# Kernel optimization log

Hardware: AMD Instinct MI355X
Metric: run time of the kernel (lower is better)

## Reference

```python
import jax, jax.numpy as jnp
import numpy as np

NUM_ITERS = 2      # num_iters default
NEG_SLOPE = 0.2    # LeakyReLU slope in GAT attention
NEG_INF = -1e9

N, E, B, H, K, L = 204800, 6144000, 4096, 8, 30, 50


def setup_inputs() -> dict:
    key = jax.random.key(0)
    ks = jax.random.split(key, 14)
    return {
        "target_features": jax.random.normal(ks[0], (N, 8), jnp.float32),
        "feature_dist_graph": jax.random.normal(ks[1], (E, 8), jnp.float32),
        "rij_dist_pairs": jax.random.uniform(ks[2], (E,), jnp.float32),
        "b_scope": jax.random.randint(ks[3], (N, K), 0, E + 1, jnp.int32),
        "start_end_env": jax.random.randint(ks[4], (N, K), 0, N + 1, jnp.int32),
        "l_scope": jax.random.randint(ks[5], (B, L), 0, N + 1, jnp.int32),
        "edge_src": jax.random.randint(ks[6], (E,), 0, N + 1, jnp.int32),
        "W_emb": jax.random.normal(ks[7], (8, H), jnp.float32),
        "b_emb": jax.random.normal(ks[8], (H,), jnp.float32),
        "W_dist": jax.random.normal(ks[9], (9, H), jnp.float32),
        "b_dist": jax.random.normal(ks[10], (H,), jnp.float32),
        "W_gat": jax.random.normal(ks[11], (H, H), jnp.float32),
        "a_src": jax.random.normal(ks[12], (H,), jnp.float32),
        "a_dst": jax.random.normal(ks[13], (H,), jnp.float32),
    }


def reference(target_features, feature_dist_graph, rij_dist_pairs,
              b_scope, start_end_env, l_scope, edge_src,
              W_emb, b_emb, W_dist, b_dist, W_gat, a_src, a_dst):
    # node embedding: [N, 8] -> [N, H]
    h = target_features @ W_emb + b_emb
    # edge (feature+distance) embedding: [E, 9] -> [E, H]
    msg = jnp.concatenate([feature_dist_graph, rij_dist_pairs[:, None]], axis=1) @ W_dist + b_dist
    zero = jnp.zeros((1, h.shape[1]), h.dtype)
    h = jnp.concatenate([zero, h], axis=0)          # zero row for 1-based / padded indices
    pad_mask = b_scope > 0                           # padded neighbor slots point at row 0
    for _ in range(NUM_ITERS):
        nbr_self = h[start_end_env]                  # getConnectedFeatures: [N, K, H] (target repeated)
        msg0 = jnp.concatenate([zero, msg], axis=0)  # zero row for padded edge indices
        nbr_msg = msg0[b_scope]                      # gathered neighbor messages [N, K, H]
        # GAT attention over the K neighbor slots
        z_s = nbr_self @ W_gat                       # [N, K, H]
        z_m = nbr_msg @ W_gat                        # [N, K, H]
        e = jax.nn.leaky_relu(z_s @ a_src + z_m @ a_dst, NEG_SLOPE)  # [N, K]
        e = jnp.where(pad_mask, e, NEG_INF)
        alpha = jax.nn.softmax(e, axis=1)            # [N, K]
        out = jnp.einsum('nk,nkh->nh', alpha, z_m)   # attention-weighted aggregate [N, H]
        h = jnp.concatenate([zero, jax.nn.elu(out)], axis=0)  # [N+1, H]
        # updateConnectedDict: scatter node states back to per-edge messages
        msg = h[edge_src]                            # [E, H]
    # readout: gather per-graph feature rows and sum -> mol_vecs [B, H]
    return h[l_scope].sum(axis=1)
```

## Files before the change

### kernel.cpp

```cpp
#include <hip/hip_runtime.h>

typedef float f32x4 __attribute__((ext_vector_type(4)));

#define NEG_SLOPE 0.2f
#define NEG_INF   -1e9f

__global__ void prep_embed(const float* __restrict__ fdg,
                           const float* __restrict__ rij,
                           const int* __restrict__ b_scope,
                           const int* __restrict__ edge_src,
                           const float* __restrict__ W_dist,
                           const float* __restrict__ b_dist,
                           const float* __restrict__ W_gat,
                           const float* __restrict__ a_src,
                           const float* __restrict__ tf,
                           const float* __restrict__ W_emb,
                           const float* __restrict__ b_emb,
                           float* __restrict__ rec,
                           int* __restrict__ src_idx,
                           float* __restrict__ h_a,
                           float* __restrict__ h_b,
                           float* __restrict__ t0,
                           float* __restrict__ t1,
                           int E, int NK, int N,
                           int nb_pair, int nb_edge, int nb_slot) {
    __shared__ float sW[72];
    __shared__ float sb[8];
    __shared__ float sWg[64];
    __shared__ float s_vec[8];
    int tid = threadIdx.x;
    int bid = blockIdx.x;

    int type, widx;
    if (bid < 2 * nb_pair) {
        type = bid & 1;
        widx = bid >> 1;
    } else {
        int r = bid - 2 * nb_pair;
        if (r < nb_edge - nb_pair)      { type = 0; widx = nb_pair + r; }
        else {
            r -= (nb_edge - nb_pair);
            if (r < nb_slot - nb_pair)  { type = 1; widx = nb_pair + r; }
            else                        { type = 2; widx = r - (nb_slot - nb_pair); }
        }
    }

    if (type == 0) {
        if (tid < 72) sW[tid] = W_dist[tid];
        else if (tid < 80) sb[tid - 72] = b_dist[tid - 72];
    } else if (type == 2) {
        if (tid < 64) sW[tid] = W_emb[tid];
        else if (tid < 72) sb[tid - 64] = b_emb[tid - 64];
        if (tid >= 128 && tid < 192) sWg[tid - 128] = W_gat[tid - 128];
    }
    __syncthreads();
    if (type == 2 && tid < 8) {
        float s = 0.f;
        #pragma unroll
        for (int j = 0; j < 8; ++j) s += sWg[tid * 8 + j] * a_src[j];
        s_vec[tid] = s;
    }
    __syncthreads();

    if (type == 0) {
        int e = widx * 256 + tid;
        if (e >= E) return;
        const f32x4* fr = reinterpret_cast<const f32x4*>(fdg + (size_t)e * 8);
        f32x4 g0 = fr[0], g1 = fr[1];
        float rv = rij[e];
        float msg[8];
        #pragma unroll
        for (int j = 0; j < 8; ++j) {
            float s = sb[j];
            #pragma unroll
            for (int i = 0; i < 4; ++i) s += g0[i] * sW[i * 8 + j];
            #pragma unroll
            for (int i = 0; i < 4; ++i) s += g1[i] * sW[(4 + i) * 8 + j];
            s += rv * sW[64 + j];
            msg[j] = s;
        }
        f32x4* op = reinterpret_cast<f32x4*>(rec + (size_t)e * 8);
        f32x4 m0 = {msg[0], msg[1], msg[2], msg[3]};
        f32x4 m1 = {msg[4], msg[5], msg[6], msg[7]};
        op[0] = m0; op[1] = m1;
    } else if (type == 1) {
        int s = widx * 256 + tid;
        if (s >= NK) return;
        int bs = b_scope[s];
        src_idx[s] = (bs > 0) ? edge_src[bs - 1] : -1;
    } else {
        int n = widx * 256 + tid;
        if (n >= N) return;
        if (n == 0) {
            #pragma unroll
            for (int j = 0; j < 8; ++j) { h_a[j] = 0.f; h_b[j] = 0.f; }
            t0[0] = 0.f;
            t1[0] = 0.f;
        }
        const f32x4* tfr = reinterpret_cast<const f32x4*>(tf + (size_t)n * 8);
        f32x4 a = tfr[0], b = tfr[1];
        float x[8] = {a[0], a[1], a[2], a[3], b[0], b[1], b[2], b[3]};
        float out[8];
        #pragma unroll
        for (int j = 0; j < 8; ++j) out[j] = sb[j];
        #pragma unroll
        for (int i = 0; i < 8; ++i)
            #pragma unroll
            for (int j = 0; j < 8; ++j)
                out[j] += x[i] * sW[i * 8 + j];
        float t = 0.f;
        #pragma unroll
        for (int p = 0; p < 8; ++p) t += out[p] * s_vec[p];
        t0[n + 1] = t;
        f32x4* hr = reinterpret_cast<f32x4*>(h_a + (size_t)(n + 1) * 8);
        f32x4 o0 = {out[0], out[1], out[2], out[3]};
        f32x4 o1 = {out[4], out[5], out[6], out[7]};
        hr[0] = o0;
        hr[1] = o1;
    }
}

__device__ __forceinline__ void finish_node(const float msg[8], float t_se, float em,
                                            bool has, bool vk, int lane, int node,
                                            const float* __restrict__ sWg,
                                            const float* __restrict__ s_as,
                                            float* __restrict__ h_next,
                                            float* __restrict__ t_next) {
    float ee = t_se + em;
    ee = (ee >= 0.f) ? ee : NEG_SLOPE * ee;
    float e = has ? ee : (vk ? NEG_INF : -3e38f);

    float m = e;
    #pragma unroll
    for (int off = 16; off; off >>= 1) m = fmaxf(m, __shfl_xor(m, off, 32));
    float p = vk ? expf(e - m) : 0.f;
    float denom = p;
    #pragma unroll
    for (int off = 16; off; off >>= 1) denom += __shfl_xor(denom, off, 32);
    float alpha = p / denom;

    float agg[8];
    #pragma unroll
    for (int j = 0; j < 8; ++j) agg[j] = alpha * msg[j];
    #pragma unroll
    for (int off = 16; off; off >>= 1)
        #pragma unroll
        for (int j = 0; j < 8; ++j) agg[j] += __shfl_xor(agg[j], off, 32);

    if (lane < 8) {
        float o = 0.f;
        #pragma unroll
        for (int i = 0; i < 8; ++i) o += agg[i] * sWg[i * 8 + lane];
        o = (o > 0.f) ? o : (expf(o) - 1.f);
        h_next[(size_t)(node + 1) * 8 + lane] = o;
        if (t_next) {
            float tv = o * s_as[lane];
            tv += __shfl_xor(tv, 1, 32);
            tv += __shfl_xor(tv, 2, 32);
            tv += __shfl_xor(tv, 4, 32);
            if (lane == 0) t_next[node + 1] = tv;
        }
    }
}

__global__ void gat_iter1_rec(const float* __restrict__ t0,
                              float* __restrict__ h1,
                              float* __restrict__ t1,
                              const int* __restrict__ b_scope,
                              const int* __restrict__ se_env,
                              const float* __restrict__ rec,
                              const float* __restrict__ W_gat,
                              const float* __restrict__ a_src,
                              const float* __restrict__ a_dst,
                              int N, int K) {
    __shared__ float sWg[64];
    __shared__ float s_as[8];
    __shared__ float s_ad[8];
    int tid = threadIdx.x;
    if (tid < 64) sWg[tid] = W_gat[tid];
    __syncthreads();
    if (tid < 8) {
        float s = 0.f;
        #pragma unroll
        for (int j = 0; j < 8; ++j) s += sWg[tid * 8 + j] * a_src[j];
        s_as[tid] = s;
    } else if (tid < 16) {
        int i = tid - 8;
        float s = 0.f;
        #pragma unroll
        for (int j = 0; j < 8; ++j) s += sWg[i * 8 + j] * a_dst[j];
        s_ad[i] = s;
    }
    __syncthreads();

    int node = blockIdx.x * 8 + (tid >> 5);
    int lane = tid & 31;
    if (node >= N) return;
    bool vk = (lane < K);

    int bs = 0, se = 0;
    if (vk) {
        bs = b_scope[(size_t)node * K + lane];
        se = se_env[(size_t)node * K + lane];
    }
    bool has = vk && (bs > 0);
    float t_se = vk ? t0[se] : 0.f;

    f32x4 m0 = {0,0,0,0}, m1 = {0,0,0,0};
    if (has) {
        const f32x4* rp = reinterpret_cast<const f32x4*>(rec + (size_t)(bs - 1) * 8);
        m0 = rp[0]; m1 = rp[1];
    }
    float msg[8] = {m0[0], m0[1], m0[2], m0[3], m1[0], m1[1], m1[2], m1[3]};
    float em = 0.f;
    #pragma unroll
    for (int j = 0; j < 8; ++j) em += msg[j] * s_ad[j];

    finish_node(msg, t_se, em, has, vk, lane, node, sWg, s_as, h1, t1);
}

__global__ void gat_iter1_fb(const float* __restrict__ t0,
                             float* __restrict__ h1,
                             float* __restrict__ t1,
                             const int* __restrict__ b_scope,
                             const int* __restrict__ se_env,
                             const float* __restrict__ fdg,
                             const float* __restrict__ rij,
                             const float* __restrict__ W_dist,
                             const float* __restrict__ b_dist,
                             const float* __restrict__ W_gat,
                             const float* __restrict__ a_src,
                             const float* __restrict__ a_dst,
                             int N, int K) {
    __shared__ float sWg[64];
    __shared__ float s_as[8];
    __shared__ float s_ad[8];
    __shared__ float sWd[72];
    __shared__ float sbd[8];
    int tid = threadIdx.x;
    if (tid < 64) sWg[tid] = W_gat[tid];
    if (tid >= 64 && tid < 136) sWd[tid - 64] = W_dist[tid - 64];
    if (tid >= 136 && tid < 144) sbd[tid - 136] = b_dist[tid - 136];
    __syncthreads();
    if (tid < 8) {
        float s = 0.f;
        #pragma unroll
        for (int j = 0; j < 8; ++j) s += sWg[tid * 8 + j] * a_src[j];
        s_as[tid] = s;
    } else if (tid < 16) {
        int i = tid - 8;
        float s = 0.f;
        #pragma unroll
        for (int j = 0; j < 8; ++j) s += sWg[i * 8 + j] * a_dst[j];
        s_ad[i] = s;
    }
    __syncthreads();

    int node = blockIdx.x * 8 + (tid >> 5);
    int lane = tid & 31;
    if (node >= N) return;
    bool vk = (lane < K);

    int bs = 0, se = 0;
    if (vk) {
        bs = b_scope[(size_t)node * K + lane];
        se = se_env[(size_t)node * K + lane];
    }
    bool has = vk && (bs > 0);
    float t_se = vk ? t0[se] : 0.f;

    float msg[8];
    #pragma unroll
    for (int j = 0; j < 8; ++j) msg[j] = 0.f;
    float em = 0.f;
    if (has) {
        const f32x4* fr = reinterpret_cast<const f32x4*>(fdg + (size_t)(bs - 1) * 8);
        f32x4 g0 = fr[0], g1 = fr[1];
        float rv = rij[bs - 1];
        #pragma unroll
        for (int j = 0; j < 8; ++j) {
            float s = sbd[j];
            #pragma unroll
            for (int i = 0; i < 4; ++i) s += g0[i] * sWd[i * 8 + j];
            #pragma unroll
            for (int i = 0; i < 4; ++i) s += g1[i] * sWd[(4 + i) * 8 + j];
            s += rv * sWd[64 + j];
            msg[j] = s;
        }
        #pragma unroll
        for (int j = 0; j < 8; ++j) em += msg[j] * s_ad[j];
    }
    finish_node(msg, t_se, em, has, vk, lane, node, sWg, s_as, h1, t1);
}

template <bool SRCIDX>
__global__ void gat_iter2(const float* __restrict__ h1,
                          const float* __restrict__ t1,
                          float* __restrict__ h2,
                          const int* __restrict__ src_idx,
                          const int* __restrict__ b_scope,
                          const int* __restrict__ se_env,
                          const int* __restrict__ edge_src,
                          const float* __restrict__ W_gat,
                          const float* __restrict__ a_dst,
                          int N, int K) {
    __shared__ float sWg[64];
    __shared__ float s_ad[8];
    int tid = threadIdx.x;
    if (tid < 64) sWg[tid] = W_gat[tid];
    __syncthreads();
    if (tid < 8) {
        float s = 0.f;
        #pragma unroll
        for (int j = 0; j < 8; ++j) s += sWg[tid * 8 + j] * a_dst[j];
        s_ad[tid] = s;
    }
    __syncthreads();

    int lane = tid & 31;
    int g = blockIdx.x * 8 + (tid >> 5);
    int nA = g * 2, nB = g * 2 + 1;
    if (nA >= N) return;
    bool hasBn = (nB < N);
    bool vk = (lane < K);

    int srcA = -1, srcB = -1, seA = 0, seB = 0;
    if (SRCIDX) {
        if (vk) {
            srcA = src_idx[(size_t)nA * K + lane];
            seA  = se_env[(size_t)nA * K + lane];
            if (hasBn) {
                srcB = src_idx[(size_t)nB * K + lane];
                seB  = se_env[(size_t)nB * K + lane];
            }
        }
    } else {
        int bsA = 0, bsB = 0;
        if (vk) {
            bsA = b_scope[(size_t)nA * K + lane];
            seA = se_env[(size_t)nA * K + lane];
            if (hasBn) {
                bsB = b_scope[(size_t)nB * K + lane];
                seB = se_env[(size_t)nB * K + lane];
            }
        }
        if (vk && bsA > 0) srcA = edge_src[bsA - 1];
        if (vk && hasBn && bsB > 0) srcB = edge_src[bsB - 1];
    }
    bool hasA = vk && (srcA >= 0);
    bool hasB = vk && hasBn && (srcB >= 0);

    float tA = vk ? t1[seA] : 0.f;
    float tB = (vk && hasBn) ? t1[seB] : 0.f;

    f32x4 a0 = {0,0,0,0}, a1 = {0,0,0,0}, b0 = {0,0,0,0}, b1 = {0,0,0,0};
    if (hasA) {
        const f32x4* mr = reinterpret_cast<const f32x4*>(h1 + (size_t)srcA * 8);
        a0 = mr[0]; a1 = mr[1];
    }
    if (hasB) {
        const f32x4* mr = reinterpret_cast<const f32x4*>(h1 + (size_t)srcB * 8);
        b0 = mr[0]; b1 = mr[1];
    }

    float msgA[8] = {a0[0], a0[1], a0[2], a0[3], a1[0], a1[1], a1[2], a1[3]};
    float emA = 0.f;
    #pragma unroll
    for (int j = 0; j < 8; ++j) emA += msgA[j] * s_ad[j];
    finish_node(msgA, tA, emA, hasA, vk, lane, nA, sWg, nullptr, h2, nullptr);
    if (hasBn) {
        float msgB[8] = {b0[0], b0[1], b0[2], b0[3], b1[0], b1[1], b1[2], b1[3]};
        float emB = 0.f;
        #pragma unroll
        for (int j = 0; j < 8; ++j) emB += msgB[j] * s_ad[j];
        finish_node(msgB, tB, emB, hasB, vk, lane, nB, sWg, nullptr, h2, nullptr);
    }
}

__global__ void readout_kernel(const float* __restrict__ h,
                               const int* __restrict__ l_scope,
                               float* __restrict__ out, int B, int L) {
    int gid = blockIdx.x * blockDim.x + threadIdx.x;
    int b = gid >> 3;
    int j = gid & 7;
    if (b >= B) return;
    float s = 0.f;
    for (int l = 0; l < L; ++l) {
        int idx = l_scope[(size_t)b * L + l];
        s += h[(size_t)idx * 8 + j];
    }
    out[(size_t)b * 8 + j] = s;
}

extern "C" void kernel_launch(void* const* d_in, const int* in_sizes, int n_in,
                              void* d_out, int out_size, void* d_ws, size_t ws_size,
                              hipStream_t stream) {
    const float* tf      = (const float*)d_in[0];
    const float* fdg     = (const float*)d_in[1];
    const float* rij     = (const float*)d_in[2];
    const int* b_scope   = (const int*)d_in[3];
    const int* start_env = (const int*)d_in[4];
    const int* l_scope   = (const int*)d_in[5];
    const int* edge_src  = (const int*)d_in[6];
    const float* W_emb   = (const float*)d_in[7];
    const float* b_emb   = (const float*)d_in[8];
    const float* W_dist  = (const float*)d_in[9];
    const float* b_dist  = (const float*)d_in[10];
    const float* W_gat   = (const float*)d_in[11];
    const float* a_src   = (const float*)d_in[12];
    const float* a_dst   = (const float*)d_in[13];
    float* out = (float*)d_out;

    const int N = in_sizes[0] / 8;
    const int E = in_sizes[1] / 8;
    const int K = in_sizes[3] / N;
    const int L = 50;
    const int B = in_sizes[5] / L;
    const int NK = N * K;

    size_t rec_f = (size_t)E * 8;
    size_t need  = (rec_f + (size_t)NK
                    + 2 * (size_t)(N + 1) * 8 + 2 * (size_t)(N + 1)) * 4;
    bool use_rec = (ws_size >= need);

    float* base = (float*)d_ws;
    float* rec  = base;
    size_t off  = use_rec ? rec_f : 0;
    float* h_a  = base + off;  off += (size_t)(N + 1) * 8;
    float* h_b  = base + off;  off += (size_t)(N + 1) * 8;
    float* t0v  = base + off;  off += (size_t)(N + 1);
    float* t1v  = base + off;  off += (size_t)(N + 1);
    int* src_idx = (int*)(base + off);

    const int nb_edge = (E + 255) / 256;
    const int nb_slot = (NK + 255) / 256;
    const int nb_node = (N + 255) / 256;
    const int nb_pair = (nb_edge < nb_slot) ? nb_edge : nb_slot;

    if (use_rec) {
        const int grid = nb_edge + nb_slot + nb_node;
        prep_embed<<<grid, 256, 0, stream>>>(
            fdg, rij, b_scope, edge_src, W_dist, b_dist, W_gat, a_src,
            tf, W_emb, b_emb, rec, src_idx, h_a, h_b, t0v, t1v,
            E, NK, N, nb_pair, nb_edge, nb_slot);
        gat_iter1_rec<<<(N + 7) / 8, 256, 0, stream>>>(t0v, h_b, t1v,
                                                       b_scope, start_env, rec,
                                                       W_gat, a_src, a_dst, N, K);
        const int g2_blocks = ((N + 1) / 2 + 7) / 8;
        gat_iter2<true><<<g2_blocks, 256, 0, stream>>>(h_b, t1v, h_a,
                                                       src_idx, b_scope, start_env,
                                                       edge_src, W_gat, a_dst, N, K);
    } else {
        prep_embed<<<nb_node, 256, 0, stream>>>(
            fdg, rij, b_scope, edge_src, W_dist, b_dist, W_gat, a_src,
            tf, W_emb, b_emb, rec, (int*)rec, h_a, h_b, t0v, t1v,
            0, 0, N, 0, 0, 0);
        gat_iter1_fb<<<(N + 7) / 8, 256, 0, stream>>>(t0v, h_b, t1v,
                                                      b_scope, start_env,
                                                      fdg, rij,
                                                      W_dist, b_dist, W_gat,
                                                      a_src, a_dst, N, K);
        const int g2_blocks = ((N + 1) / 2 + 7) / 8;
        gat_iter2<false><<<g2_blocks, 256, 0, stream>>>(h_b, t1v, h_a,
                                                        (const int*)rec, b_scope, start_env,
                                                        edge_src, W_gat, a_dst, N, K);
    }

    readout_kernel<<<(B * 8 + 255) / 256, 256, 0, stream>>>(h_a, l_scope, out, B, L);
}
```

Measured before the change: 406.8 us.

## Split each neighbor slot across two lanes in a 64-wide wavefront per node

The GAT iteration kernels now use a full 64-lane wavefront per node, with two lanes per neighbor slot. Each lane loads one 16-byte half of the gathered 8-float message row, and the halves are exchanged with a shuffle. The aim is to spread the random gather loads across more lanes and to use wave64 natively instead of 32-lane sub-groups. In exchange, the reductions gain an extra shuffle step, half the lanes do duplicate softmax work, and the two-nodes-per-warp batching in iteration 2 is dropped.

```diff
diff --git a/kernel.cpp b/kernel.cpp
--- a/kernel.cpp
+++ b/kernel.cpp
@@ -120,45 +120,45 @@
     }
 }
 
-__device__ __forceinline__ void finish_node(const float msg[8], float t_se, float em,
-                                            bool has, bool vk, int lane, int node,
+__device__ __forceinline__ void finish_pair(const float msg[8], float t_se, float em,
+                                            bool own, bool has, int k, int h, int node,
                                             const float* __restrict__ sWg,
                                             const float* __restrict__ s_as,
                                             float* __restrict__ h_next,
                                             float* __restrict__ t_next) {
     float ee = t_se + em;
     ee = (ee >= 0.f) ? ee : NEG_SLOPE * ee;
-    float e = has ? ee : (vk ? NEG_INF : -3e38f);
+    float e = own ? (has ? ee : NEG_INF) : -3e38f;
 
     float m = e;
     #pragma unroll
-    for (int off = 16; off; off >>= 1) m = fmaxf(m, __shfl_xor(m, off, 32));
-    float p = vk ? expf(e - m) : 0.f;
+    for (int off = 32; off >= 2; off >>= 1) m = fmaxf(m, __shfl_xor(m, off, 64));
+    float p = own ? expf(e - m) : 0.f;
     float denom = p;
     #pragma unroll
-    for (int off = 16; off; off >>= 1) denom += __shfl_xor(denom, off, 32);
+    for (int off = 32; off >= 2; off >>= 1) denom += __shfl_xor(denom, off, 64);
     float alpha = p / denom;
 
     float agg[8];
     #pragma unroll
     for (int j = 0; j < 8; ++j) agg[j] = alpha * msg[j];
     #pragma unroll
-    for (int off = 16; off; off >>= 1)
-        #pragma unroll
-        for (int j = 0; j < 8; ++j) agg[j] += __shfl_xor(agg[j], off, 32);
-
-    if (lane < 8) {
+    for (int off = 32; off >= 2; off >>= 1)
+        #pragma unroll
+        for (int j = 0; j < 8; ++j) agg[j] += __shfl_xor(agg[j], off, 64);
+
+    if (h == 0 && k < 8) {
         float o = 0.f;
         #pragma unroll
-        for (int i = 0; i < 8; ++i) o += agg[i] * sWg[i * 8 + lane];
+        for (int i = 0; i < 8; ++i) o += agg[i] * sWg[i * 8 + k];
         o = (o > 0.f) ? o : (expf(o) - 1.f);
-        h_next[(size_t)(node + 1) * 8 + lane] = o;
+        h_next[(size_t)(node + 1) * 8 + k] = o;
         if (t_next) {
-            float tv = o * s_as[lane];
-            tv += __shfl_xor(tv, 1, 32);
-            tv += __shfl_xor(tv, 2, 32);
-            tv += __shfl_xor(tv, 4, 32);
-            if (lane == 0) t_next[node + 1] = tv;
+            float tv = o * s_as[k];
+            tv += __shfl_xor(tv, 2, 64);
+            tv += __shfl_xor(tv, 4, 64);
+            tv += __shfl_xor(tv, 8, 64);
+            if (k == 0) t_next[node + 1] = tv;
         }
     }
 }
@@ -193,30 +193,132 @@
     }
     __syncthreads();
 
-    int node = blockIdx.x * 8 + (tid >> 5);
-    int lane = tid & 31;
+    int node = blockIdx.x * 4 + (tid >> 6);
+    int lane = tid & 63;
+    int k = lane >> 1;
+    int h = lane & 1;
     if (node >= N) return;
-    bool vk = (lane < K);
+    bool vk  = (k < K);
+    bool own = vk && (h == 0);
 
     int bs = 0, se = 0;
     if (vk) {
-        bs = b_scope[(size_t)node * K + lane];
-        se = se_env[(size_t)node * K + lane];
+        bs = b_scope[(size_t)node * K + k];
+        se = se_env[(size_t)node * K + k];
     }
     bool has = vk && (bs > 0);
-    float t_se = vk ? t0[se] : 0.f;
-
-    f32x4 m0 = {0,0,0,0}, m1 = {0,0,0,0};
-    if (has) {
-        const f32x4* rp = reinterpret_cast<const f32x4*>(rec + (size_t)(bs - 1) * 8);
-        m0 = rp[0]; m1 = rp[1];
-    }
-    float msg[8] = {m0[0], m0[1], m0[2], m0[3], m1[0], m1[1], m1[2], m1[3]};
+
+    f32x4 mh = {0, 0, 0, 0};
+    if (has)
+        mh = *reinterpret_cast<const f32x4*>(rec + (size_t)(bs - 1) * 8 + h * 4);
+    float t_se = own ? t0[se] : 0.f;
+
+    f32x4 m1;
+    #pragma unroll
+    for (int c = 0; c < 4; ++c) m1[c] = __shfl(mh[c], lane | 1, 64);
+    float msg[8] = {mh[0], mh[1], mh[2], mh[3], m1[0], m1[1], m1[2], m1[3]};
+
     float em = 0.f;
     #pragma unroll
     for (int j = 0; j < 8; ++j) em += msg[j] * s_ad[j];
 
-    finish_node(msg, t_se, em, has, vk, lane, node, sWg, s_as, h1, t1);
+    finish_pair(msg, t_se, em, own, has, k, h, node, sWg, s_as, h1, t1);
+}
+
+__global__ void gat_iter2_pair(const float* __restrict__ h1,
+                               const float* __restrict__ t1,
+                               float* __restrict__ h2,
+                               const int* __restrict__ src_idx,
+                               const int* __restrict__ se_env,
+                               const float* __restrict__ W_gat,
+                               const float* __restrict__ a_dst,
+                               int N, int K) {
+    __shared__ float sWg[64];
+    __shared__ float s_ad[8];
+    int tid = threadIdx.x;
+    if (tid < 64) sWg[tid] = W_gat[tid];
+    __syncthreads();
+    if (tid < 8) {
+        float s = 0.f;
+        #pragma unroll
+        for (int j = 0; j < 8; ++j) s += sWg[tid * 8 + j] * a_dst[j];
+        s_ad[tid] = s;
+    }
+    __syncthreads();
+
+    int node = blockIdx.x * 4 + (tid >> 6);
+    int lane = tid & 63;
+    int k = lane >> 1;
+    int h = lane & 1;
+    if (node >= N) return;
+    bool vk  = (k < K);
+    bool own = vk && (h == 0);
+
+    int src = -1, se = 0;
+    if (vk) {
+        src = src_idx[(size_t)node * K + k];
+        se  = se_env[(size_t)node * K + k];
+    }
+    bool has = vk && (src >= 0);
+
+    f32x4 mh = {0, 0, 0, 0};
+    if (has)
+        mh = *reinterpret_cast<const f32x4*>(h1 + (size_t)src * 8 + h * 4);
+    float t_se = own ? t1[se] : 0.f;
+
+    f32x4 m1;
+    #pragma unroll
+    for (int c = 0; c < 4; ++c) m1[c] = __shfl(mh[c], lane | 1, 64);
+    float msg[8] = {mh[0], mh[1], mh[2], mh[3], m1[0], m1[1], m1[2], m1[3]};
+
+    float em = 0.f;
+    #pragma unroll
+    for (int j = 0; j < 8; ++j) em += msg[j] * s_ad[j];
+
+    finish_pair(msg, t_se, em, own, has, k, h, node, sWg, nullptr, h2, nullptr);
+}
+
+__device__ __forceinline__ void finish_node(const float msg[8], float t_se, float em,
+                                            bool has, bool vk, int lane, int node,
+                                            const float* __restrict__ sWg,
+                                            const float* __restrict__ s_as,
+                                            float* __restrict__ h_next,
+                                            float* __restrict__ t_next) {
+    float ee = t_se + em;
+    ee = (ee >= 0.f) ? ee : NEG_SLOPE * ee;
+    float e = has ? ee : (vk ? NEG_INF : -3e38f);
+
+    float m = e;
+    #pragma unroll
+    for (int off = 16; off; off >>= 1) m = fmaxf(m, __shfl_xor(m, off, 32));
+    float p = vk ? expf(e - m) : 0.f;
+    float denom = p;
+    #pragma unroll
+    for (int off = 16; off; off >>= 1) denom += __shfl_xor(denom, off, 32);
+    float alpha = p / denom;
+
+    float agg[8];
+    #pragma unroll
+    for (int j = 0; j < 8; ++j) agg[j] = alpha * msg[j];
+    #pragma unroll
+    for (int off = 16; off; off >>= 1)
+        #pragma unroll
+        for (int j = 0; j < 8; ++j) agg[j] += __shfl_xor(agg[j], off, 32);
+
+    if (lane < 8) {
+        float o = 0.f;
+        #pragma unroll
+        for (int i = 0; i < 8; ++i) o += agg[i] * sWg[i * 8 + lane];
+        o = (o > 0.f) ? o : (expf(o) - 1.f);
+        h_next[(size_t)(node + 1) * 8 + lane] = o;
+        if (t_next) {
+            float tv = o * s_as[lane];
+            tv += __shfl_xor(tv, 1, 32);
+            tv += __shfl_xor(tv, 2, 32);
+            tv += __shfl_xor(tv, 4, 32);
+            if (lane == 0) t_next[node + 1] = tv;
+        }
+    }
 }
 
 __global__ void gat_iter1_fb(const float* __restrict__ t0,
@@ -293,17 +395,15 @@
     finish_node(msg, t_se, em, has, vk, lane, node, sWg, s_as, h1, t1);
 }
 
-template <bool SRCIDX>
-__global__ void gat_iter2(const float* __restrict__ h1,
-                          const float* __restrict__ t1,
-                          float* __restrict__ h2,
-                          const int* __restrict__ src_idx,
-                          const int* __restrict__ b_scope,
-                          const int* __restrict__ se_env,
-                          const int* __restrict__ edge_src,
-                          const float* __restrict__ W_gat,
-                          const float* __restrict__ a_dst,
-                          int N, int K) {
+__global__ void gat_iter2_fb(const float* __restrict__ h1,
+                             const float* __restrict__ t1,
+                             float* __restrict__ h2,
+                             const int* __restrict__ b_scope,
+                             const int* __restrict__ se_env,
+                             const int* __restrict__ edge_src,
+                             const float* __restrict__ W_gat,
+                             const float* __restrict__ a_dst,
+                             int N, int K) {
     __shared__ float sWg[64];
     __shared__ float s_ad[8];
     int tid = threadIdx.x;
@@ -317,64 +417,34 @@
     }
     __syncthreads();
 
+    int node = blockIdx.x * 8 + (tid >> 5);
     int lane = tid & 31;
-    int g = blockIdx.x * 8 + (tid >> 5);
-    int nA = g * 2, nB = g * 2 + 1;
-    if (nA >= N) return;
-    bool hasBn = (nB < N);
+    if (node >= N) return;
     bool vk = (lane < K);
 
-    int srcA = -1, srcB = -1, seA = 0, seB = 0;
-    if (SRCIDX) {
-        if (vk) {
-            srcA = src_idx[(size_t)nA * K + lane];
-            seA  = se_env[(size_t)nA * K + lane];
-            if (hasBn) {
-                srcB = src_idx[(size_t)nB * K + lane];
-                seB  = se_env[(size_t)nB * K + lane];
-            }
-        }
-    } else {
-        int bsA = 0, bsB = 0;
-        if (vk) {
-            bsA = b_scope[(size_t)nA * K + lane];
-            seA = se_env[(size_t)nA * K + lane];
-            if (hasBn) {
-                bsB = b_scope[(size_t)nB * K + lane];
-                seB = se_env[(size_t)nB * K + lane];
-            }
-        }
-        if (vk && bsA > 0) srcA = edge_src[bsA - 1];
-        if (vk && hasBn && bsB > 0) srcB = edge_src[bsB - 1];
-    }
-    bool hasA = vk && (srcA >= 0);
-    bool hasB = vk && hasBn && (srcB >= 0);
-
-    float tA = vk ? t1[seA] : 0.f;
-    float tB = (vk && hasBn) ? t1[seB] : 0.f;
-
-    f32x4 a0 = {0,0,0,0}, a1 = {0,0,0,0}, b0 = {0,0,0,0}, b1 = {0,0,0,0};
-    if (hasA) {
-        const f32x4* mr = reinterpret_cast<const f32x4*>(h1 + (size_t)srcA * 8);
-        a0 = mr[0]; a1 = mr[1];
-    }
-    if (hasB) {
-        const f32x4* mr = reinterpret_cast<const f32x4*>(h1 + (size_t)srcB * 8);
-        b0 = mr[0]; b1 = mr[1];
-    }
-
-    float msgA[8] = {a0[0], a0[1], a0[2], a0[3], a1[0], a1[1], a1[2], a1[3]};
-    float emA = 0.f;
-    #pragma unroll
-    for (int j = 0; j < 8; ++j) emA += msgA[j] * s_ad[j];
-    finish_node(msgA, tA, emA, hasA, vk, lane, nA, sWg, nullptr, h2, nullptr);
-    if (hasBn) {
-        float msgB[8] = {b0[0], b0[1], b0[2], b0[3], b1[0], b1[1], b1[2], b1[3]};
-        float emB = 0.f;
-        #pragma unroll
-        for (int j = 0; j < 8; ++j) emB += msgB[j] * s_ad[j];
-        finish_node(msgB, tB, emB, hasB, vk, lane, nB, sWg, nullptr, h2, nullptr);
-    }
+    int bs = 0, se = 0;
+    if (vk) {
+        bs = b_scope[(size_t)node * K + lane];
+        se = se_env[(size_t)node * K + lane];
+    }
+    int src = -1;
+    if (vk && bs > 0) src = edge_src[bs - 1];
+    bool has = vk && (src >= 0);
+    float t_se = vk ? t1[se] : 0.f;
+
+    float msg[8];
+    #pragma unroll
+    for (int j = 0; j < 8; ++j) msg[j] = 0.f;
+    if (has) {
+        const f32x4* mr = reinterpret_cast<const f32x4*>(h1 + (size_t)src * 8);
+        f32x4 m0 = mr[0], m1 = mr[1];
+        msg[0] = m0[0]; msg[1] = m0[1]; msg[2] = m0[2]; msg[3] = m0[3];
+        msg[4] = m1[0]; msg[5] = m1[1]; msg[6] = m1[2]; msg[7] = m1[3];
+    }
+    float em = 0.f;
+    #pragma unroll
+    for (int j = 0; j < 8; ++j) em += msg[j] * s_ad[j];
+    finish_node(msg, t_se, em, has, vk, lane, node, sWg, nullptr, h2, nullptr);
 }
 
 __global__ void readout_kernel(const float* __restrict__ h,
@@ -438,18 +508,16 @@
     const int nb_pair = (nb_edge < nb_slot) ? nb_edge : nb_slot;
 
     if (use_rec) {
-        const int grid = nb_edge + nb_slot + nb_node;
-        prep_embed<<<grid, 256, 0, stream>>>(
+        prep_embed<<<nb_edge + nb_slot + nb_node, 256, 0, stream>>>(
             fdg, rij, b_scope, edge_src, W_dist, b_dist, W_gat, a_src,
             tf, W_emb, b_emb, rec, src_idx, h_a, h_b, t0v, t1v,
             E, NK, N, nb_pair, nb_edge, nb_slot);
-        gat_iter1_rec<<<(N + 7) / 8, 256, 0, stream>>>(t0v, h_b, t1v,
+        gat_iter1_rec<<<(N + 3) / 4, 256, 0, stream>>>(t0v, h_b, t1v,
                                                        b_scope, start_env, rec,
                                                        W_gat, a_src, a_dst, N, K);
-        const int g2_blocks = ((N + 1) / 2 + 7) / 8;
-        gat_iter2<true><<<g2_blocks, 256, 0, stream>>>(h_b, t1v, h_a,
-                                                       src_idx, b_scope, start_env,
-                                                       edge_src, W_gat, a_dst, N, K);
+        gat_iter2_pair<<<(N + 3) / 4, 256, 0, stream>>>(h_b, t1v, h_a,
+                                                        src_idx, start_env,
+                                                        W_gat, a_dst, N, K);
     } else {
         prep_embed<<<nb_node, 256, 0, stream>>>(
             fdg, rij, b_scope, edge_src, W_dist, b_dist, W_gat, a_src,
@@ -460,10 +528,9 @@
                                                       fdg, rij,
                                                       W_dist, b_dist, W_gat,
                                                       a_src, a_dst, N, K);
-        const int g2_blocks = ((N + 1) / 2 + 7) / 8;
-        gat_iter2<false><<<g2_blocks, 256, 0, stream>>>(h_b, t1v, h_a,
-                                                        (const int*)rec, b_scope, start_env,
-                                                        edge_src, W_gat, a_dst, N, K);
+        gat_iter2_fb<<<(N + 7) / 8, 256, 0, stream>>>(h_b, t1v, h_a,
+                                                      b_scope, start_env,
+                                                      edge_src, W_gat, a_dst, N, K);
     }
 
     readout_kernel<<<(B * 8 + 255) / 256, 256, 0, stream>>>(h_a, l_scope, out, B, L);
```

Measured after the change: 474.9 us. 16.8% more time.
